# Kernel tuning notes

Measured on AMD Instinct MI355X. Metric: run time of the kernel, lower is better.

## Reference

```python
import jax, jax.numpy as jnp
import numpy as np

LN_EPS = 1e-5


def setup_inputs() -> dict:
    key = jax.random.key(0)
    ks = jax.random.split(key, 5)
    dim, hidden = 512, 8
    B, S = 128, 1024
    x = jax.random.normal(ks[0], (B, S, dim), dtype=jnp.float32)
    # torch Linear: weight [out, in], bias [out]
    w1 = jax.random.normal(ks[1], (hidden, dim), dtype=jnp.float32) * (1.0 / np.sqrt(dim))
    b1 = jax.random.normal(ks[2], (hidden,), dtype=jnp.float32) * 0.02
    w2 = jax.random.normal(ks[3], (dim, hidden), dtype=jnp.float32) * (1.0 / np.sqrt(hidden))
    b2 = jax.random.normal(ks[4], (dim,), dtype=jnp.float32) * 0.02
    gamma = jnp.ones((dim,), dtype=jnp.float32)
    beta = jnp.zeros((dim,), dtype=jnp.float32)
    return {"x": x, "w1": w1, "b1": b1, "w2": w2, "b2": b2,
            "gamma": gamma, "beta": beta}


def _layernorm(y, gamma, beta):
    mu = jnp.mean(y, axis=-1, keepdims=True)
    var = jnp.mean(jnp.square(y - mu), axis=-1, keepdims=True)
    return (y - mu) * jax.lax.rsqrt(var + LN_EPS) * gamma + beta


def reference(x, w1, b1, w2, b2, gamma, beta):
    # y = gelu(gelu(LN(x) @ W1^T + b1) @ W2^T + b2) + x  (exact erf GELU, as torch nn.GELU default)
    y = _layernorm(x, gamma, beta)                       # [B,S,D]
    h = jnp.einsum('bsd,hd->bsh', y, w1) + b1            # [B,S,8]
    h = jax.nn.gelu(h, approximate=False)
    o = jnp.einsum('bsh,dh->bsd', h, w2) + b2            # [B,S,D]
    o = jax.nn.gelu(o, approximate=False)
    return o + x
```

## Files before the change

### kernel.cpp

```cpp
#include <hip/hip_runtime.h>
#include <math.h>

#define DIM 512
#define HID 8
#define LN_EPS 1e-5f

typedef float f32x4 __attribute__((ext_vector_type(4)));

#define DPP_XOR1 0xB1
#define DPP_XOR2 0x4E
#define DPP_HM   0x141
#define DPP_ROR8 0x128
#define DPP_ROR4 0x124

template <int CTRL>
__device__ __forceinline__ float dpp_movf(float v) {
    int r = __builtin_amdgcn_update_dpp(0, __builtin_bit_cast(int, v),
                                        CTRL, 0xF, 0xF, true);
    return __builtin_bit_cast(float, r);
}
template <int CTRL>
__device__ __forceinline__ float dpp_addf(float v) {
    return v + dpp_movf<CTRL>(v);
}
__device__ __forceinline__ float readlanef(float v, int lane) {
    return __builtin_bit_cast(float,
        __builtin_amdgcn_readlane(__builtin_bit_cast(int, v), lane));
}

__device__ __forceinline__ float gelu_fast(float v) {
    const float C = 0.044715f;
    const float K = 2.30258819f;
    float v2 = v * v;
    float t  = v * fmaf(C, v2, 1.0f);
    float e  = __builtin_amdgcn_exp2f(K * t);
    float r  = __builtin_amdgcn_rcpf(e + 1.0f);
    return fmaf(-v, r, v);
}

__device__ __forceinline__ void load8(float* dst, const float* __restrict__ src) {
    const f32x4* p = reinterpret_cast<const f32x4*>(src);
    f32x4 a = p[0];
    f32x4 b = p[1];
    dst[0] = a.x; dst[1] = a.y; dst[2] = a.z; dst[3] = a.w;
    dst[4] = b.x; dst[5] = b.y; dst[6] = b.z; dst[7] = b.w;
}

__global__ __launch_bounds__(256, 2)
void mlp_fused_kernel(const float* __restrict__ x,
                      const float* __restrict__ w1,
                      const float* __restrict__ b1,
                      const float* __restrict__ w2,
                      const float* __restrict__ b2,
                      const float* __restrict__ gamma,
                      const float* __restrict__ beta,
                      float* __restrict__ out,
                      int nrows, int rows_per_wave) {
    const int lane  = threadIdx.x & 63;
    const int widx  = threadIdx.x >> 6;
    const int wgid  = blockIdx.x * 4 + widx;
    const int dbase = lane * 8;
    const int lj    = lane & 7;

    const int r0 = wgid * rows_per_wave;
    if (r0 >= nrows) return;
    int r1 = r0 + rows_per_wave;
    if (r1 > nrows) r1 = nrows;

    float w1r[64];
#pragma unroll
    for (int j = 0; j < HID; ++j)
        load8(&w1r[j * 8], w1 + j * DIM + dbase);

    float w2p[64];
#pragma unroll
    for (int k = 0; k < 8; ++k)
#pragma unroll
        for (int t = 0; t < 8; ++t)
            w2p[k * 8 + t] = w2[(size_t)(dbase + k) * HID + (lj ^ t)];

    float gm[8], bt[8], b2r[8];
    load8(gm,  gamma + dbase);
    load8(bt,  beta  + dbase);
    load8(b2r, b2    + dbase);
    const float b1own = b1[lj];

    float xv[8];
    load8(xv, x + (size_t)r0 * DIM + dbase);

    for (int r = r0; r < r1; ++r) {
#pragma unroll
        for (int i = 0; i < 64; ++i) asm volatile("" : "+v"(w1r[i]));
#pragma unroll
        for (int i = 0; i < 64; ++i) asm volatile("" : "+v"(w2p[i]));
#pragma unroll
        for (int i = 0; i < 8; ++i) {
            asm volatile("" : "+v"(gm[i]));
            asm volatile("" : "+v"(bt[i]));
            asm volatile("" : "+v"(b2r[i]));
        }

        float xn[8];
        const int rn = (r + 1 < r1) ? (r + 1) : r;
        load8(xn, x + (size_t)rn * DIM + dbase);

        float s = 0.f, q = 0.f;
#pragma unroll
        for (int k = 0; k < 8; ++k) { s += xv[k]; q = fmaf(xv[k], xv[k], q); }
        s = dpp_addf<DPP_XOR1>(s); q = dpp_addf<DPP_XOR1>(q);
        s = dpp_addf<DPP_XOR2>(s); q = dpp_addf<DPP_XOR2>(q);
        s = dpp_addf<DPP_HM  >(s); q = dpp_addf<DPP_HM  >(q);
        s = dpp_addf<DPP_ROR8>(s); q = dpp_addf<DPP_ROR8>(q);
        const float stot = (readlanef(s, 0) + readlanef(s, 16))
                         + (readlanef(s, 32) + readlanef(s, 48));
        const float qtot = (readlanef(q, 0) + readlanef(q, 16))
                         + (readlanef(q, 32) + readlanef(q, 48));
        const float mu  = stot * (1.0f / DIM);
        const float var = qtot * (1.0f / DIM) - mu * mu;
        const float rs  = rsqrtf(var + LN_EPS);

        float y[8];
#pragma unroll
        for (int k = 0; k < 8; ++k)
            y[k] = fmaf((xv[k] - mu) * rs, gm[k], bt[k]);

        float ph[8] = {0.f, 0.f, 0.f, 0.f, 0.f, 0.f, 0.f, 0.f};
#pragma unroll
        for (int j = 0; j < HID; ++j)
#pragma unroll
            for (int k = 0; k < 8; ++k)
                ph[j] = fmaf(y[k], w1r[j * 8 + k], ph[j]);

#pragma unroll
        for (int j = 0; j < HID; ++j) ph[j] = dpp_addf<DPP_XOR1>(ph[j]);
#pragma unroll
        for (int j = 0; j < HID; ++j) ph[j] = dpp_addf<DPP_XOR2>(ph[j]);
#pragma unroll
        for (int j = 0; j < HID; ++j) ph[j] = dpp_addf<DPP_HM>(ph[j]);

        float sel = ph[0];
        sel = (lj == 1) ? ph[1] : sel;
        sel = (lj == 2) ? ph[2] : sel;
        sel = (lj == 3) ? ph[3] : sel;
        sel = (lj == 4) ? ph[4] : sel;
        sel = (lj == 5) ? ph[5] : sel;
        sel = (lj == 6) ? ph[6] : sel;
        sel = (lj == 7) ? ph[7] : sel;

        sel = dpp_addf<DPP_ROR8>(sel);
        sel += __shfl_xor(sel, 16, 64);
        sel += __shfl_xor(sel, 32, 64);

        const float hact = gelu_fast(sel + b1own);

        float hj[8];
        hj[0] = hact;
        hj[1] = dpp_movf<DPP_XOR1>(hj[0]);
        hj[2] = dpp_movf<DPP_XOR2>(hj[0]);
        hj[3] = dpp_movf<DPP_XOR2>(hj[1]);
        hj[4] = dpp_movf<DPP_ROR4>(hj[0]);
        hj[5] = dpp_movf<DPP_ROR4>(hj[1]);
        hj[6] = dpp_movf<DPP_ROR4>(hj[2]);
        hj[7] = dpp_movf<DPP_ROR4>(hj[3]);

        float ov[8];
#pragma unroll
        for (int k = 0; k < 8; ++k) {
            float o = b2r[k];
#pragma unroll
            for (int t = 0; t < 8; ++t)
                o = fmaf(hj[t], w2p[k * 8 + t], o);
            ov[k] = gelu_fast(o) + xv[k];
        }

        float* po = out + (size_t)r * DIM + dbase;
        f32x4 v0 = {ov[0], ov[1], ov[2], ov[3]};
        f32x4 v1 = {ov[4], ov[5], ov[6], ov[7]};
        __builtin_nontemporal_store(v0, reinterpret_cast<f32x4*>(po));
        __builtin_nontemporal_store(v1, reinterpret_cast<f32x4*>(po) + 1);

#pragma unroll
        for (int k = 0; k < 8; ++k) xv[k] = xn[k];
    }
}

extern "C" void kernel_launch(void* const* d_in, const int* in_sizes, int n_in,
                              void* d_out, int out_size, void* d_ws, size_t ws_size,
                              hipStream_t stream) {
    const float* x     = (const float*)d_in[0];
    const float* w1    = (const float*)d_in[1];
    const float* b1    = (const float*)d_in[2];
    const float* w2    = (const float*)d_in[3];
    const float* b2    = (const float*)d_in[4];
    const float* gamma = (const float*)d_in[5];
    const float* beta  = (const float*)d_in[6];
    float* out = (float*)d_out;

    const int nrows = in_sizes[0] / DIM;
    const int blocks = 2048;
    const int total_waves = blocks * 4;
    const int rows_per_wave = (nrows + total_waves - 1) / total_waves;

    mlp_fused_kernel<<<blocks, 256, 0, stream>>>(
        x, w1, b1, w2, b2, gamma, beta, out, nrows, rows_per_wave);
}
```

Measured before the change: 118.8 us.

## Fold LayerNorm into W1 and split each row across two waves

```diff
diff --git a/kernel.cpp b/kernel.cpp
--- a/kernel.cpp
+++ b/kernel.cpp
@@ -11,7 +11,6 @@
 #define DPP_XOR2 0x4E
 #define DPP_HM   0x141
 #define DPP_ROR8 0x128
-#define DPP_ROR4 0x124
 
 template <int CTRL>
 __device__ __forceinline__ float dpp_movf(float v) {
@@ -38,15 +37,37 @@
     return fmaf(-v, r, v);
 }
 
-__device__ __forceinline__ void load8(float* dst, const float* __restrict__ src) {
-    const f32x4* p = reinterpret_cast<const f32x4*>(src);
-    f32x4 a = p[0];
-    f32x4 b = p[1];
-    dst[0] = a.x; dst[1] = a.y; dst[2] = a.z; dst[3] = a.w;
-    dst[4] = b.x; dst[5] = b.y; dst[6] = b.z; dst[7] = b.w;
-}
-
-__global__ __launch_bounds__(256, 2)
+__device__ __forceinline__ float reduce8(float ph[8], int lj) {
+#pragma unroll
+    for (int j = 0; j < 8; ++j) ph[j] = dpp_addf<DPP_XOR1>(ph[j]);
+#pragma unroll
+    for (int j = 0; j < 8; ++j) ph[j] = dpp_addf<DPP_XOR2>(ph[j]);
+#pragma unroll
+    for (int j = 0; j < 8; ++j) ph[j] = dpp_addf<DPP_HM>(ph[j]);
+    float sel = ph[0];
+    sel = (lj == 1) ? ph[1] : sel;
+    sel = (lj == 2) ? ph[2] : sel;
+    sel = (lj == 3) ? ph[3] : sel;
+    sel = (lj == 4) ? ph[4] : sel;
+    sel = (lj == 5) ? ph[5] : sel;
+    sel = (lj == 6) ? ph[6] : sel;
+    sel = (lj == 7) ? ph[7] : sel;
+    sel = dpp_addf<DPP_ROR8>(sel);
+    sel += __shfl_xor(sel, 16, 64);
+    sel += __shfl_xor(sel, 32, 64);
+    return sel;
+}
+
+__device__ __forceinline__ float wave_sum(float v) {
+    v = dpp_addf<DPP_XOR1>(v);
+    v = dpp_addf<DPP_XOR2>(v);
+    v = dpp_addf<DPP_HM>(v);
+    v = dpp_addf<DPP_ROR8>(v);
+    return (readlanef(v, 0) + readlanef(v, 16))
+         + (readlanef(v, 32) + readlanef(v, 48));
+}
+
+__global__ __launch_bounds__(128, 4)
 void mlp_fused_kernel(const float* __restrict__ x,
                       const float* __restrict__ w1,
                       const float* __restrict__ b1,
@@ -55,132 +76,120 @@
                       const float* __restrict__ gamma,
                       const float* __restrict__ beta,
                       float* __restrict__ out,
-                      int nrows, int rows_per_wave) {
-    const int lane  = threadIdx.x & 63;
-    const int widx  = threadIdx.x >> 6;
-    const int wgid  = blockIdx.x * 4 + widx;
-    const int dbase = lane * 8;
-    const int lj    = lane & 7;
-
-    const int r0 = wgid * rows_per_wave;
+                      int nrows, int rows_per_block) {
+    __shared__ float lds[96];
+
+    const int tid  = threadIdx.x;
+    const int lane = tid & 63;
+    const int w    = tid >> 6;
+    const int lj   = lane & 7;
+    const int dbase = w * 256 + lane * 4;
+
+    const int r0 = blockIdx.x * rows_per_block;
     if (r0 >= nrows) return;
-    int r1 = r0 + rows_per_wave;
+    int r1 = r0 + rows_per_block;
     if (r1 > nrows) r1 = nrows;
 
-    float w1r[64];
-#pragma unroll
-    for (int j = 0; j < HID; ++j)
-        load8(&w1r[j * 8], w1 + j * DIM + dbase);
-
-    float w2p[64];
-#pragma unroll
-    for (int k = 0; k < 8; ++k)
-#pragma unroll
-        for (int t = 0; t < 8; ++t)
-            w2p[k * 8 + t] = w2[(size_t)(dbase + k) * HID + (lj ^ t)];
-
-    float gm[8], bt[8], b2r[8];
-    load8(gm,  gamma + dbase);
-    load8(bt,  beta  + dbase);
-    load8(b2r, b2    + dbase);
-    const float b1own = b1[lj];
-
-    float xv[8];
-    load8(xv, x + (size_t)r0 * DIM + dbase);
+    f32x4 gmv = *reinterpret_cast<const f32x4*>(gamma + dbase);
+    f32x4 btv = *reinterpret_cast<const f32x4*>(beta  + dbase);
+
+    float w1g[32];
+    float c1p[8], w1sp[8];
+#pragma unroll
+    for (int j = 0; j < 8; ++j) { c1p[j] = 0.f; w1sp[j] = 0.f; }
+#pragma unroll
+    for (int j = 0; j < 8; ++j) {
+        f32x4 raw = *reinterpret_cast<const f32x4*>(w1 + j * DIM + dbase);
+#pragma unroll
+        for (int k = 0; k < 4; ++k) {
+            float rw = raw[k];
+            c1p[j] = fmaf(btv[k], rw, c1p[j]);
+            float wg = rw * gmv[k];
+            w1g[j * 4 + k] = wg;
+            w1sp[j] += wg;
+        }
+    }
+    float w1sw = reduce8(w1sp, lj);
+    float c1w  = reduce8(c1p, lj);
+    if (lane < 8) {
+        lds[64 + w * 8 + lj] = w1sw;
+        lds[80 + w * 8 + lj] = c1w;
+    }
+    __syncthreads();
+    const float W1s = lds[64 + lj] + lds[72 + lj];
+    const float b1e = b1[lj] + lds[80 + lj] + lds[88 + lj];
+
+    float w2n[32];
+#pragma unroll
+    for (int k = 0; k < 4; ++k) {
+        f32x4 lo = *reinterpret_cast<const f32x4*>(w2 + (size_t)(dbase + k) * HID);
+        f32x4 hi = *reinterpret_cast<const f32x4*>(w2 + (size_t)(dbase + k) * HID + 4);
+#pragma unroll
+        for (int j = 0; j < 4; ++j) { w2n[k * 8 + j] = lo[j]; w2n[k * 8 + 4 + j] = hi[j]; }
+    }
+    f32x4 b2v = *reinterpret_cast<const f32x4*>(b2 + dbase);
+
+    f32x4 xv = *reinterpret_cast<const f32x4*>(x + (size_t)r0 * DIM + dbase);
 
     for (int r = r0; r < r1; ++r) {
-#pragma unroll
-        for (int i = 0; i < 64; ++i) asm volatile("" : "+v"(w1r[i]));
-#pragma unroll
-        for (int i = 0; i < 64; ++i) asm volatile("" : "+v"(w2p[i]));
-#pragma unroll
-        for (int i = 0; i < 8; ++i) {
-            asm volatile("" : "+v"(gm[i]));
-            asm volatile("" : "+v"(bt[i]));
-            asm volatile("" : "+v"(b2r[i]));
-        }
-
-        float xn[8];
         const int rn = (r + 1 < r1) ? (r + 1) : r;
-        load8(xn, x + (size_t)rn * DIM + dbase);
+        f32x4 xn = *reinterpret_cast<const f32x4*>(x + (size_t)rn * DIM + dbase);
 
         float s = 0.f, q = 0.f;
 #pragma unroll
-        for (int k = 0; k < 8; ++k) { s += xv[k]; q = fmaf(xv[k], xv[k], q); }
-        s = dpp_addf<DPP_XOR1>(s); q = dpp_addf<DPP_XOR1>(q);
-        s = dpp_addf<DPP_XOR2>(s); q = dpp_addf<DPP_XOR2>(q);
-        s = dpp_addf<DPP_HM  >(s); q = dpp_addf<DPP_HM  >(q);
-        s = dpp_addf<DPP_ROR8>(s); q = dpp_addf<DPP_ROR8>(q);
-        const float stot = (readlanef(s, 0) + readlanef(s, 16))
-                         + (readlanef(s, 32) + readlanef(s, 48));
-        const float qtot = (readlanef(q, 0) + readlanef(q, 16))
-                         + (readlanef(q, 32) + readlanef(q, 48));
+        for (int k = 0; k < 4; ++k) { s += xv[k]; q = fmaf(xv[k], xv[k], q); }
+
+        float ph[8];
+#pragma unroll
+        for (int j = 0; j < 8; ++j) {
+            float a = 0.f;
+#pragma unroll
+            for (int k = 0; k < 4; ++k)
+                a = fmaf(xv[k], w1g[j * 4 + k], a);
+            ph[j] = a;
+        }
+
+        const float sw = wave_sum(s);
+        const float qw = wave_sum(q);
+        const float Hw = reduce8(ph, lj);
+
+        const int base = (r & 1) * 32;
+        if (lane == 0) {
+            lds[base + w * 2 + 0] = sw;
+            lds[base + w * 2 + 1] = qw;
+        }
+        if (lane < 8) lds[base + 4 + w * 8 + lj] = Hw;
+        __syncthreads();
+
+        const float stot = lds[base + 0] + lds[base + 2];
+        const float qtot = lds[base + 1] + lds[base + 3];
+        const float Sx   = lds[base + 4 + lj] + lds[base + 12 + lj];
+
         const float mu  = stot * (1.0f / DIM);
         const float var = qtot * (1.0f / DIM) - mu * mu;
         const float rs  = rsqrtf(var + LN_EPS);
 
-        float y[8];
-#pragma unroll
-        for (int k = 0; k < 8; ++k)
-            y[k] = fmaf((xv[k] - mu) * rs, gm[k], bt[k]);
-
-        float ph[8] = {0.f, 0.f, 0.f, 0.f, 0.f, 0.f, 0.f, 0.f};
-#pragma unroll
-        for (int j = 0; j < HID; ++j)
-#pragma unroll
-            for (int k = 0; k < 8; ++k)
-                ph[j] = fmaf(y[k], w1r[j * 8 + k], ph[j]);
-
-#pragma unroll
-        for (int j = 0; j < HID; ++j) ph[j] = dpp_addf<DPP_XOR1>(ph[j]);
-#pragma unroll
-        for (int j = 0; j < HID; ++j) ph[j] = dpp_addf<DPP_XOR2>(ph[j]);
-#pragma unroll
-        for (int j = 0; j < HID; ++j) ph[j] = dpp_addf<DPP_HM>(ph[j]);
-
-        float sel = ph[0];
-        sel = (lj == 1) ? ph[1] : sel;
-        sel = (lj == 2) ? ph[2] : sel;
-        sel = (lj == 3) ? ph[3] : sel;
-        sel = (lj == 4) ? ph[4] : sel;
-        sel = (lj == 5) ? ph[5] : sel;
-        sel = (lj == 6) ? ph[6] : sel;
-        sel = (lj == 7) ? ph[7] : sel;
-
-        sel = dpp_addf<DPP_ROR8>(sel);
-        sel += __shfl_xor(sel, 16, 64);
-        sel += __shfl_xor(sel, 32, 64);
-
-        const float hact = gelu_fast(sel + b1own);
-
-        float hj[8];
-        hj[0] = hact;
-        hj[1] = dpp_movf<DPP_XOR1>(hj[0]);
-        hj[2] = dpp_movf<DPP_XOR2>(hj[0]);
-        hj[3] = dpp_movf<DPP_XOR2>(hj[1]);
-        hj[4] = dpp_movf<DPP_ROR4>(hj[0]);
-        hj[5] = dpp_movf<DPP_ROR4>(hj[1]);
-        hj[6] = dpp_movf<DPP_ROR4>(hj[2]);
-        hj[7] = dpp_movf<DPP_ROR4>(hj[3]);
-
-        float ov[8];
-#pragma unroll
-        for (int k = 0; k < 8; ++k) {
-            float o = b2r[k];
-#pragma unroll
-            for (int t = 0; t < 8; ++t)
-                o = fmaf(hj[t], w2p[k * 8 + t], o);
+        const float t  = fmaf(-mu, W1s, Sx);
+        const float vH = gelu_fast(fmaf(rs, t, b1e));
+
+        float sH[8];
+#pragma unroll
+        for (int j = 0; j < 8; ++j) sH[j] = readlanef(vH, j);
+
+        f32x4 ov;
+#pragma unroll
+        for (int k = 0; k < 4; ++k) {
+            float o = b2v[k];
+#pragma unroll
+            for (int j = 0; j < 8; ++j)
+                o = fmaf(sH[j], w2n[k * 8 + j], o);
             ov[k] = gelu_fast(o) + xv[k];
         }
 
-        float* po = out + (size_t)r * DIM + dbase;
-        f32x4 v0 = {ov[0], ov[1], ov[2], ov[3]};
-        f32x4 v1 = {ov[4], ov[5], ov[6], ov[7]};
-        __builtin_nontemporal_store(v0, reinterpret_cast<f32x4*>(po));
-        __builtin_nontemporal_store(v1, reinterpret_cast<f32x4*>(po) + 1);
-
-#pragma unroll
-        for (int k = 0; k < 8; ++k) xv[k] = xn[k];
+        __builtin_nontemporal_store(
+            ov, reinterpret_cast<f32x4*>(out + (size_t)r * DIM + dbase));
+
+        xv = xn;
     }
 }
 
@@ -196,11 +205,10 @@
     const float* beta  = (const float*)d_in[6];
     float* out = (float*)d_out;
 
-    const int nrows = in_sizes[0] / DIM;
-    const int blocks = 2048;
-    const int total_waves = blocks * 4;
-    const int rows_per_wave = (nrows + total_waves - 1) / total_waves;
-
-    mlp_fused_kernel<<<blocks, 256, 0, stream>>>(
-        x, w1, b1, w2, b2, gamma, beta, out, nrows, rows_per_wave);
-}
+    const int nrows  = in_sizes[0] / DIM;
+    const int blocks = 4096;
+    const int rows_per_block = (nrows + blocks - 1) / blocks;
+
+    mlp_fused_kernel<<<blocks, 128, 0, stream>>>(
+        x, w1, b1, w2, b2, gamma, beta, out, nrows, rows_per_block);
+}
```

Measured after the change: 148.3 us. +24.8%, slower.

## Fold LayerNorm affine into W1 and process two rows per iteration

Applied to the files above, without the earlier changes.

```diff
diff --git a/kernel.cpp b/kernel.cpp
--- a/kernel.cpp
+++ b/kernel.cpp
@@ -38,6 +38,36 @@
     return fmaf(-v, r, v);
 }
 
+__device__ __forceinline__ float wave_sum(float v) {
+    v = dpp_addf<DPP_XOR1>(v);
+    v = dpp_addf<DPP_XOR2>(v);
+    v = dpp_addf<DPP_HM>(v);
+    v = dpp_addf<DPP_ROR8>(v);
+    return (readlanef(v, 0) + readlanef(v, 16))
+         + (readlanef(v, 32) + readlanef(v, 48));
+}
+
+__device__ __forceinline__ float reduce8(float ph[8], int lj) {
+#pragma unroll
+    for (int j = 0; j < 8; ++j) ph[j] = dpp_addf<DPP_XOR1>(ph[j]);
+#pragma unroll
+    for (int j = 0; j < 8; ++j) ph[j] = dpp_addf<DPP_XOR2>(ph[j]);
+#pragma unroll
+    for (int j = 0; j < 8; ++j) ph[j] = dpp_addf<DPP_HM>(ph[j]);
+    float sel = ph[0];
+    sel = (lj == 1) ? ph[1] : sel;
+    sel = (lj == 2) ? ph[2] : sel;
+    sel = (lj == 3) ? ph[3] : sel;
+    sel = (lj == 4) ? ph[4] : sel;
+    sel = (lj == 5) ? ph[5] : sel;
+    sel = (lj == 6) ? ph[6] : sel;
+    sel = (lj == 7) ? ph[7] : sel;
+    sel = dpp_addf<DPP_ROR8>(sel);
+    sel += __shfl_xor(sel, 16, 64);
+    sel += __shfl_xor(sel, 32, 64);
+    return sel;
+}
+
 __device__ __forceinline__ void load8(float* dst, const float* __restrict__ src) {
     const f32x4* p = reinterpret_cast<const f32x4*>(src);
     f32x4 a = p[0];
@@ -46,7 +76,8 @@
     dst[4] = b.x; dst[5] = b.y; dst[6] = b.z; dst[7] = b.w;
 }
 
-__global__ __launch_bounds__(256, 2)
+__global__ __launch_bounds__(256)
+__attribute__((amdgpu_waves_per_eu(2, 2)))
 void mlp_fused_kernel(const float* __restrict__ x,
                       const float* __restrict__ w1,
                       const float* __restrict__ b1,
@@ -57,8 +88,8 @@
                       float* __restrict__ out,
                       int nrows, int rows_per_wave) {
     const int lane  = threadIdx.x & 63;
-    const int widx  = threadIdx.x >> 6;
-    const int wgid  = blockIdx.x * 4 + widx;
+    const int wav   = threadIdx.x >> 6;
+    const int wgid  = blockIdx.x * 4 + wav;
     const int dbase = lane * 8;
     const int lj    = lane & 7;
 
@@ -67,10 +98,28 @@
     int r1 = r0 + rows_per_wave;
     if (r1 > nrows) r1 = nrows;
 
-    float w1r[64];
-#pragma unroll
-    for (int j = 0; j < HID; ++j)
-        load8(&w1r[j * 8], w1 + j * DIM + dbase);
+    float gm[8], bt[8];
+    load8(gm, gamma + dbase);
+    load8(bt, beta  + dbase);
+
+    float w1g[64];
+    float w1sp[8], c1p[8];
+#pragma unroll
+    for (int j = 0; j < 8; ++j) { w1sp[j] = 0.f; c1p[j] = 0.f; }
+#pragma unroll
+    for (int j = 0; j < 8; ++j) {
+        float raw[8];
+        load8(raw, w1 + j * DIM + dbase);
+#pragma unroll
+        for (int k = 0; k < 8; ++k) {
+            c1p[j] = fmaf(bt[k], raw[k], c1p[j]);
+            float wg = raw[k] * gm[k];
+            w1g[j * 8 + k] = wg;
+            w1sp[j] += wg;
+        }
+    }
+    const float W1s = reduce8(w1sp, lj);
+    const float b1e = b1[lj] + reduce8(c1p, lj);
 
     float w2p[64];
 #pragma unroll
@@ -79,82 +128,133 @@
         for (int t = 0; t < 8; ++t)
             w2p[k * 8 + t] = w2[(size_t)(dbase + k) * HID + (lj ^ t)];
 
-    float gm[8], bt[8], b2r[8];
-    load8(gm,  gamma + dbase);
-    load8(bt,  beta  + dbase);
-    load8(b2r, b2    + dbase);
-    const float b1own = b1[lj];
-
-    float xv[8];
-    load8(xv, x + (size_t)r0 * DIM + dbase);
-
-    for (int r = r0; r < r1; ++r) {
-#pragma unroll
-        for (int i = 0; i < 64; ++i) asm volatile("" : "+v"(w1r[i]));
-#pragma unroll
-        for (int i = 0; i < 64; ++i) asm volatile("" : "+v"(w2p[i]));
-#pragma unroll
-        for (int i = 0; i < 8; ++i) {
-            asm volatile("" : "+v"(gm[i]));
-            asm volatile("" : "+v"(bt[i]));
-            asm volatile("" : "+v"(b2r[i]));
-        }
-
-        float xn[8];
-        const int rn = (r + 1 < r1) ? (r + 1) : r;
-        load8(xn, x + (size_t)rn * DIM + dbase);
-
+    float b2r[8];
+    load8(b2r, b2 + dbase);
+
+    float xvA[8], xvB[8];
+    load8(xvA, x + (size_t)r0 * DIM + dbase);
+    {
+        int rb = (r0 + 1 < r1) ? r0 + 1 : r0;
+        load8(xvB, x + (size_t)rb * DIM + dbase);
+    }
+
+    int r = r0;
+    for (; r + 1 < r1; r += 2) {
+        float xnA[8], xnB[8];
+        const int ra2 = (r + 2 < r1) ? r + 2 : r1 - 1;
+        const int rb2 = (r + 3 < r1) ? r + 3 : r1 - 1;
+        load8(xnA, x + (size_t)ra2 * DIM + dbase);
+        load8(xnB, x + (size_t)rb2 * DIM + dbase);
+
+        float sA = 0.f, qA = 0.f, sB = 0.f, qB = 0.f;
+#pragma unroll
+        for (int k = 0; k < 8; ++k) {
+            sA += xvA[k]; qA = fmaf(xvA[k], xvA[k], qA);
+            sB += xvB[k]; qB = fmaf(xvB[k], xvB[k], qB);
+        }
+        float phA[8], phB[8];
+#pragma unroll
+        for (int j = 0; j < 8; ++j) {
+            float a = 0.f, b = 0.f;
+#pragma unroll
+            for (int k = 0; k < 8; ++k) {
+                a = fmaf(xvA[k], w1g[j * 8 + k], a);
+                b = fmaf(xvB[k], w1g[j * 8 + k], b);
+            }
+            phA[j] = a; phB[j] = b;
+        }
+
+        const float swA = wave_sum(sA);
+        const float qwA = wave_sum(qA);
+        const float swB = wave_sum(sB);
+        const float qwB = wave_sum(qB);
+        const float HwA = reduce8(phA, lj);
+        const float HwB = reduce8(phB, lj);
+
+        const float muA  = swA * (1.0f / DIM);
+        const float varA = qwA * (1.0f / DIM) - muA * muA;
+        const float rsA  = rsqrtf(varA + LN_EPS);
+        const float hA   = gelu_fast(fmaf(rsA, fmaf(-muA, W1s, HwA), b1e));
+        float hjA[8];
+        hjA[0] = hA;
+        hjA[1] = dpp_movf<DPP_XOR1>(hjA[0]);
+        hjA[2] = dpp_movf<DPP_XOR2>(hjA[0]);
+        hjA[3] = dpp_movf<DPP_XOR2>(hjA[1]);
+        hjA[4] = dpp_movf<DPP_ROR4>(hjA[0]);
+        hjA[5] = dpp_movf<DPP_ROR4>(hjA[1]);
+        hjA[6] = dpp_movf<DPP_ROR4>(hjA[2]);
+        hjA[7] = dpp_movf<DPP_ROR4>(hjA[3]);
+        f32x4 oA0, oA1;
+#pragma unroll
+        for (int k = 0; k < 8; ++k) {
+            float o = b2r[k];
+#pragma unroll
+            for (int t = 0; t < 8; ++t)
+                o = fmaf(hjA[t], w2p[k * 8 + t], o);
+            float val = gelu_fast(o) + xvA[k];
+            if (k < 4) oA0[k] = val; else oA1[k - 4] = val;
+        }
+        {
+            float* po = out + (size_t)r * DIM + dbase;
+            __builtin_nontemporal_store(oA0, reinterpret_cast<f32x4*>(po));
+            __builtin_nontemporal_store(oA1, reinterpret_cast<f32x4*>(po) + 1);
+        }
+
+        const float muB  = swB * (1.0f / DIM);
+        const float varB = qwB * (1.0f / DIM) - muB * muB;
+        const float rsB  = rsqrtf(varB + LN_EPS);
+        const float hB   = gelu_fast(fmaf(rsB, fmaf(-muB, W1s, HwB), b1e));
+        float hjB[8];
+        hjB[0] = hB;
+        hjB[1] = dpp_movf<DPP_XOR1>(hjB[0]);
+        hjB[2] = dpp_movf<DPP_XOR2>(hjB[0]);
+        hjB[3] = dpp_movf<DPP_XOR2>(hjB[1]);
+        hjB[4] = dpp_movf<DPP_ROR4>(hjB[0]);
+        hjB[5] = dpp_movf<DPP_ROR4>(hjB[1]);
+        hjB[6] = dpp_movf<DPP_ROR4>(hjB[2]);
+        hjB[7] = dpp_movf<DPP_ROR4>(hjB[3]);
+        f32x4 oB0, oB1;
+#pragma unroll
+        for (int k = 0; k < 8; ++k) {
+            float o = b2r[k];
+#pragma unroll
+            for (int t = 0; t < 8; ++t)
+                o = fmaf(hjB[t], w2p[k * 8 + t], o);
+            float val = gelu_fast(o) + xvB[k];
+            if (k < 4) oB0[k] = val; else oB1[k - 4] = val;
+        }
+        {
+            float* po = out + (size_t)(r + 1) * DIM + dbase;
+            __builtin_nontemporal_store(oB0, reinterpret_cast<f32x4*>(po));
+            __builtin_nontemporal_store(oB1, reinterpret_cast<f32x4*>(po) + 1);
+        }
+
+#pragma unroll
+        for (int k = 0; k < 8; ++k) { xvA[k] = xnA[k]; xvB[k] = xnB[k]; }
+    }
+
+    if (r < r1) {
         float s = 0.f, q = 0.f;
 #pragma unroll
-        for (int k = 0; k < 8; ++k) { s += xv[k]; q = fmaf(xv[k], xv[k], q); }
-        s = dpp_addf<DPP_XOR1>(s); q = dpp_addf<DPP_XOR1>(q);
-        s = dpp_addf<DPP_XOR2>(s); q = dpp_addf<DPP_XOR2>(q);
-        s = dpp_addf<DPP_HM  >(s); q = dpp_addf<DPP_HM  >(q);
-        s = dpp_addf<DPP_ROR8>(s); q = dpp_addf<DPP_ROR8>(q);
-        const float stot = (readlanef(s, 0) + readlanef(s, 16))
-                         + (readlanef(s, 32) + readlanef(s, 48));
-        const float qtot = (readlanef(q, 0) + readlanef(q, 16))
-                         + (readlanef(q, 32) + readlanef(q, 48));
-        const float mu  = stot * (1.0f / DIM);
-        const float var = qtot * (1.0f / DIM) - mu * mu;
+        for (int k = 0; k < 8; ++k) { s += xvA[k]; q = fmaf(xvA[k], xvA[k], q); }
+        float ph[8];
+#pragma unroll
+        for (int j = 0; j < 8; ++j) {
+            float a = 0.f;
+#pragma unroll
+            for (int k = 0; k < 8; ++k)
+                a = fmaf(xvA[k], w1g[j * 8 + k], a);
+            ph[j] = a;
+        }
+        const float sw = wave_sum(s);
+        const float qw = wave_sum(q);
+        const float Hw = reduce8(ph, lj);
+        const float mu  = sw * (1.0f / DIM);
+        const float var = qw * (1.0f / DIM) - mu * mu;
         const float rs  = rsqrtf(var + LN_EPS);
-
-        float y[8];
-#pragma unroll
-        for (int k = 0; k < 8; ++k)
-            y[k] = fmaf((xv[k] - mu) * rs, gm[k], bt[k]);
-
-        float ph[8] = {0.f, 0.f, 0.f, 0.f, 0.f, 0.f, 0.f, 0.f};
-#pragma unroll
-        for (int j = 0; j < HID; ++j)
-#pragma unroll
-            for (int k = 0; k < 8; ++k)
-                ph[j] = fmaf(y[k], w1r[j * 8 + k], ph[j]);
-
-#pragma unroll
-        for (int j = 0; j < HID; ++j) ph[j] = dpp_addf<DPP_XOR1>(ph[j]);
-#pragma unroll
-        for (int j = 0; j < HID; ++j) ph[j] = dpp_addf<DPP_XOR2>(ph[j]);
-#pragma unroll
-        for (int j = 0; j < HID; ++j) ph[j] = dpp_addf<DPP_HM>(ph[j]);
-
-        float sel = ph[0];
-        sel = (lj == 1) ? ph[1] : sel;
-        sel = (lj == 2) ? ph[2] : sel;
-        sel = (lj == 3) ? ph[3] : sel;
-        sel = (lj == 4) ? ph[4] : sel;
-        sel = (lj == 5) ? ph[5] : sel;
-        sel = (lj == 6) ? ph[6] : sel;
-        sel = (lj == 7) ? ph[7] : sel;
-
-        sel = dpp_addf<DPP_ROR8>(sel);
-        sel += __shfl_xor(sel, 16, 64);
-        sel += __shfl_xor(sel, 32, 64);
-
-        const float hact = gelu_fast(sel + b1own);
-
+        const float h   = gelu_fast(fmaf(rs, fmaf(-mu, W1s, Hw), b1e));
         float hj[8];
-        hj[0] = hact;
+        hj[0] = h;
         hj[1] = dpp_movf<DPP_XOR1>(hj[0]);
         hj[2] = dpp_movf<DPP_XOR2>(hj[0]);
         hj[3] = dpp_movf<DPP_XOR2>(hj[1]);
@@ -162,25 +262,19 @@
         hj[5] = dpp_movf<DPP_ROR4>(hj[1]);
         hj[6] = dpp_movf<DPP_ROR4>(hj[2]);
         hj[7] = dpp_movf<DPP_ROR4>(hj[3]);
-
-        float ov[8];
+        f32x4 o0, o1;
 #pragma unroll
         for (int k = 0; k < 8; ++k) {
             float o = b2r[k];
 #pragma unroll
             for (int t = 0; t < 8; ++t)
                 o = fmaf(hj[t], w2p[k * 8 + t], o);
-            ov[k] = gelu_fast(o) + xv[k];
-        }
-
+            float val = gelu_fast(o) + xvA[k];
+            if (k < 4) o0[k] = val; else o1[k - 4] = val;
+        }
         float* po = out + (size_t)r * DIM + dbase;
-        f32x4 v0 = {ov[0], ov[1], ov[2], ov[3]};
-        f32x4 v1 = {ov[4], ov[5], ov[6], ov[7]};
-        __builtin_nontemporal_store(v0, reinterpret_cast<f32x4*>(po));
-        __builtin_nontemporal_store(v1, reinterpret_cast<f32x4*>(po) + 1);
-
-#pragma unroll
-        for (int k = 0; k < 8; ++k) xv[k] = xn[k];
+        __builtin_nontemporal_store(o0, reinterpret_cast<f32x4*>(po));
+        __builtin_nontemporal_store(o1, reinterpret_cast<f32x4*>(po) + 1);
     }
 }
 
@@ -196,8 +290,8 @@
     const float* beta  = (const float*)d_in[6];
     float* out = (float*)d_out;
 
-    const int nrows = in_sizes[0] / DIM;
-    const int blocks = 2048;
+    const int nrows  = in_sizes[0] / DIM;
+    const int blocks = 512;
     const int total_waves = blocks * 4;
     const int rows_per_wave = (nrows + total_waves - 1) / total_waves;
 
```

After: 126.9 us. +6.8%, slower.

## Fold LayerNorm affine into W1 so the hidden projection runs on raw x

Applied to the files above, without the earlier changes.

```diff
diff --git a/kernel.cpp b/kernel.cpp
--- a/kernel.cpp
+++ b/kernel.cpp
@@ -38,6 +38,36 @@
     return fmaf(-v, r, v);
 }
 
+__device__ __forceinline__ float wave_sum(float v) {
+    v = dpp_addf<DPP_XOR1>(v);
+    v = dpp_addf<DPP_XOR2>(v);
+    v = dpp_addf<DPP_HM>(v);
+    v = dpp_addf<DPP_ROR8>(v);
+    return (readlanef(v, 0) + readlanef(v, 16))
+         + (readlanef(v, 32) + readlanef(v, 48));
+}
+
+__device__ __forceinline__ float reduce8(float ph[8], int lj) {
+#pragma unroll
+    for (int j = 0; j < 8; ++j) ph[j] = dpp_addf<DPP_XOR1>(ph[j]);
+#pragma unroll
+    for (int j = 0; j < 8; ++j) ph[j] = dpp_addf<DPP_XOR2>(ph[j]);
+#pragma unroll
+    for (int j = 0; j < 8; ++j) ph[j] = dpp_addf<DPP_HM>(ph[j]);
+    float sel = ph[0];
+    sel = (lj == 1) ? ph[1] : sel;
+    sel = (lj == 2) ? ph[2] : sel;
+    sel = (lj == 3) ? ph[3] : sel;
+    sel = (lj == 4) ? ph[4] : sel;
+    sel = (lj == 5) ? ph[5] : sel;
+    sel = (lj == 6) ? ph[6] : sel;
+    sel = (lj == 7) ? ph[7] : sel;
+    sel = dpp_addf<DPP_ROR8>(sel);
+    sel += __shfl_xor(sel, 16, 64);
+    sel += __shfl_xor(sel, 32, 64);
+    return sel;
+}
+
 __device__ __forceinline__ void load8(float* dst, const float* __restrict__ src) {
     const f32x4* p = reinterpret_cast<const f32x4*>(src);
     f32x4 a = p[0];
@@ -46,7 +76,7 @@
     dst[4] = b.x; dst[5] = b.y; dst[6] = b.z; dst[7] = b.w;
 }
 
-__global__ __launch_bounds__(256, 2)
+__global__ __launch_bounds__(256)
 void mlp_fused_kernel(const float* __restrict__ x,
                       const float* __restrict__ w1,
                       const float* __restrict__ b1,
@@ -57,8 +87,8 @@
                       float* __restrict__ out,
                       int nrows, int rows_per_wave) {
     const int lane  = threadIdx.x & 63;
-    const int widx  = threadIdx.x >> 6;
-    const int wgid  = blockIdx.x * 4 + widx;
+    const int wav   = threadIdx.x >> 6;
+    const int wgid  = blockIdx.x * 4 + wav;
     const int dbase = lane * 8;
     const int lj    = lane & 7;
 
@@ -67,10 +97,28 @@
     int r1 = r0 + rows_per_wave;
     if (r1 > nrows) r1 = nrows;
 
-    float w1r[64];
-#pragma unroll
-    for (int j = 0; j < HID; ++j)
-        load8(&w1r[j * 8], w1 + j * DIM + dbase);
+    float gm[8], bt[8];
+    load8(gm, gamma + dbase);
+    load8(bt, beta  + dbase);
+
+    float w1g[64];
+    float w1sp[8], c1p[8];
+#pragma unroll
+    for (int j = 0; j < 8; ++j) { w1sp[j] = 0.f; c1p[j] = 0.f; }
+#pragma unroll
+    for (int j = 0; j < 8; ++j) {
+        float raw[8];
+        load8(raw, w1 + j * DIM + dbase);
+#pragma unroll
+        for (int k = 0; k < 8; ++k) {
+            c1p[j] = fmaf(bt[k], raw[k], c1p[j]);
+            float wg = raw[k] * gm[k];
+            w1g[j * 8 + k] = wg;
+            w1sp[j] += wg;
+        }
+    }
+    const float W1s = reduce8(w1sp, lj);
+    const float b1e = b1[lj] + reduce8(c1p, lj);
 
     float w2p[64];
 #pragma unroll
@@ -79,27 +127,13 @@
         for (int t = 0; t < 8; ++t)
             w2p[k * 8 + t] = w2[(size_t)(dbase + k) * HID + (lj ^ t)];
 
-    float gm[8], bt[8], b2r[8];
-    load8(gm,  gamma + dbase);
-    load8(bt,  beta  + dbase);
-    load8(b2r, b2    + dbase);
-    const float b1own = b1[lj];
+    float b2r[8];
+    load8(b2r, b2 + dbase);
 
     float xv[8];
     load8(xv, x + (size_t)r0 * DIM + dbase);
 
     for (int r = r0; r < r1; ++r) {
-#pragma unroll
-        for (int i = 0; i < 64; ++i) asm volatile("" : "+v"(w1r[i]));
-#pragma unroll
-        for (int i = 0; i < 64; ++i) asm volatile("" : "+v"(w2p[i]));
-#pragma unroll
-        for (int i = 0; i < 8; ++i) {
-            asm volatile("" : "+v"(gm[i]));
-            asm volatile("" : "+v"(bt[i]));
-            asm volatile("" : "+v"(b2r[i]));
-        }
-
         float xn[8];
         const int rn = (r + 1 < r1) ? (r + 1) : r;
         load8(xn, x + (size_t)rn * DIM + dbase);
@@ -107,54 +141,29 @@
         float s = 0.f, q = 0.f;
 #pragma unroll
         for (int k = 0; k < 8; ++k) { s += xv[k]; q = fmaf(xv[k], xv[k], q); }
-        s = dpp_addf<DPP_XOR1>(s); q = dpp_addf<DPP_XOR1>(q);
-        s = dpp_addf<DPP_XOR2>(s); q = dpp_addf<DPP_XOR2>(q);
-        s = dpp_addf<DPP_HM  >(s); q = dpp_addf<DPP_HM  >(q);
-        s = dpp_addf<DPP_ROR8>(s); q = dpp_addf<DPP_ROR8>(q);
-        const float stot = (readlanef(s, 0) + readlanef(s, 16))
-                         + (readlanef(s, 32) + readlanef(s, 48));
-        const float qtot = (readlanef(q, 0) + readlanef(q, 16))
-                         + (readlanef(q, 32) + readlanef(q, 48));
-        const float mu  = stot * (1.0f / DIM);
-        const float var = qtot * (1.0f / DIM) - mu * mu;
+
+        float ph[8];
+#pragma unroll
+        for (int j = 0; j < 8; ++j) {
+            float a = 0.f;
+#pragma unroll
+            for (int k = 0; k < 8; ++k)
+                a = fmaf(xv[k], w1g[j * 8 + k], a);
+            ph[j] = a;
+        }
+
+        const float sw = wave_sum(s);
+        const float qw = wave_sum(q);
+        const float Hw = reduce8(ph, lj);
+
+        const float mu  = sw * (1.0f / DIM);
+        const float var = qw * (1.0f / DIM) - mu * mu;
         const float rs  = rsqrtf(var + LN_EPS);
 
-        float y[8];
-#pragma unroll
-        for (int k = 0; k < 8; ++k)
-            y[k] = fmaf((xv[k] - mu) * rs, gm[k], bt[k]);
-
-        float ph[8] = {0.f, 0.f, 0.f, 0.f, 0.f, 0.f, 0.f, 0.f};
-#pragma unroll
-        for (int j = 0; j < HID; ++j)
-#pragma unroll
-            for (int k = 0; k < 8; ++k)
-                ph[j] = fmaf(y[k], w1r[j * 8 + k], ph[j]);
-
-#pragma unroll
-        for (int j = 0; j < HID; ++j) ph[j] = dpp_addf<DPP_XOR1>(ph[j]);
-#pragma unroll
-        for (int j = 0; j < HID; ++j) ph[j] = dpp_addf<DPP_XOR2>(ph[j]);
-#pragma unroll
-        for (int j = 0; j < HID; ++j) ph[j] = dpp_addf<DPP_HM>(ph[j]);
-
-        float sel = ph[0];
-        sel = (lj == 1) ? ph[1] : sel;
-        sel = (lj == 2) ? ph[2] : sel;
-        sel = (lj == 3) ? ph[3] : sel;
-        sel = (lj == 4) ? ph[4] : sel;
-        sel = (lj == 5) ? ph[5] : sel;
-        sel = (lj == 6) ? ph[6] : sel;
-        sel = (lj == 7) ? ph[7] : sel;
-
-        sel = dpp_addf<DPP_ROR8>(sel);
-        sel += __shfl_xor(sel, 16, 64);
-        sel += __shfl_xor(sel, 32, 64);
-
-        const float hact = gelu_fast(sel + b1own);
+        const float h = gelu_fast(fmaf(rs, fmaf(-mu, W1s, Hw), b1e));
 
         float hj[8];
-        hj[0] = hact;
+        hj[0] = h;
         hj[1] = dpp_movf<DPP_XOR1>(hj[0]);
         hj[2] = dpp_movf<DPP_XOR2>(hj[0]);
         hj[3] = dpp_movf<DPP_XOR2>(hj[1]);
@@ -163,21 +172,20 @@
         hj[6] = dpp_movf<DPP_ROR4>(hj[2]);
         hj[7] = dpp_movf<DPP_ROR4>(hj[3]);
 
-        float ov[8];
+        f32x4 o0, o1;
 #pragma unroll
         for (int k = 0; k < 8; ++k) {
             float o = b2r[k];
 #pragma unroll
             for (int t = 0; t < 8; ++t)
                 o = fmaf(hj[t], w2p[k * 8 + t], o);
-            ov[k] = gelu_fast(o) + xv[k];
+            float val = gelu_fast(o) + xv[k];
+            if (k < 4) o0[k] = val; else o1[k - 4] = val;
         }
 
         float* po = out + (size_t)r * DIM + dbase;
-        f32x4 v0 = {ov[0], ov[1], ov[2], ov[3]};
-        f32x4 v1 = {ov[4], ov[5], ov[6], ov[7]};
-        __builtin_nontemporal_store(v0, reinterpret_cast<f32x4*>(po));
-        __builtin_nontemporal_store(v1, reinterpret_cast<f32x4*>(po) + 1);
+        __builtin_nontemporal_store(o0, reinterpret_cast<f32x4*>(po));
+        __builtin_nontemporal_store(o1, reinterpret_cast<f32x4*>(po) + 1);
 
 #pragma unroll
         for (int k = 0; k < 8; ++k) xv[k] = xn[k];
@@ -196,7 +204,7 @@
     const float* beta  = (const float*)d_in[6];
     float* out = (float*)d_out;
 
-    const int nrows = in_sizes[0] / DIM;
+    const int nrows  = in_sizes[0] / DIM;
     const int blocks = 2048;
     const int total_waves = blocks * 4;
     const int rows_per_wave = (nrows + total_waves - 1) / total_waves;
```

Result: slower. 141.5 us (+19.1%).
